# Kernel optimization log

Hardware: AMD Instinct MI355X
Metric: run time of the kernel (lower is better)

The kernel has to match this reference:

```python
import jax, jax.numpy as jnp
import numpy as np

K_BITS = 128  # hash bits (k in __init__)
WORD = 32     # pack bits into uint32 words -> K_BITS // WORD = 4 words


def _pack_bits(bits_u32):
    # bits_u32: [N, K_BITS] uint32 in {0,1} -> [N, K_BITS//WORD] uint32 keys
    N = bits_u32.shape[0]
    b = bits_u32.reshape(N, K_BITS // WORD, WORD)
    shifts = jnp.arange(WORD, dtype=jnp.uint32)
    return jnp.sum(jnp.left_shift(b, shifts), axis=-1, dtype=jnp.uint32)  # [N, 4]


def setup_inputs() -> dict:
    key = jax.random.key(0)
    k1, k2 = jax.random.split(key)
    T, B, D = 128, 64, 4096
    latent_state = jax.random.normal(k1, (T, B, D), dtype=jnp.float32)
    A = jax.random.normal(k2, (K_BITS, D), dtype=jnp.float32)  # fixed random projection buffer
    return {"latent_state": latent_state, "A": A}


def reference(latent_state, A):
    # latent_state: [T, B, D]; A: [k, D]. Returns intrinsic reward [T, B].
    T, B, D = latent_state.shape
    flat = latent_state.reshape(T * B, D)                    # detach is a no-op for fwd
    proj = flat @ A.T                                        # [N, k]
    bits = (proj > 0).astype(jnp.uint32)                     # SimHash sign bits
    words = _pack_bits(bits)                                 # [N, 4] collision-free 128-bit key

    # counts dict starts empty each run: visit count of row i is the number of
    # rows j <= i with an identical key (keys processed in row order).
    N = words.shape[0]
    eq = jnp.ones((N, N), dtype=bool)
    for w in range(K_BITS // WORD):  # small fixed loop over 4 key words
        eq = eq & (words[:, None, w] == words[None, :, w])
    counts = jnp.tril(eq).sum(axis=1)                        # [N] int, >= 1
    intrinsic = 1.0 / jnp.sqrt(counts.astype(latent_state.dtype))
    return intrinsic.reshape(T, B)
```

## Files before the change

### kernel.cpp

```cpp
#include <hip/hip_runtime.h>
#include <stdint.h>

#define D_DIM 4096
#define N_ROWS 8192

typedef __attribute__((ext_vector_type(8))) short bfrag8;
typedef __attribute__((ext_vector_type(4))) float facc4;
typedef unsigned long long u64;

__device__ __forceinline__ uint32_t pack_bf16x2(float lo, float hi) {
    union { float f; uint32_t u; } a, b;
    a.f = lo; b.f = hi;
    return (b.u & 0xFFFF0000u) | (a.u >> 16);
}

__global__ void __launch_bounds__(256)
prep_A(const float* __restrict__ A, uint32_t* __restrict__ A_sw) {
    const int S = blockIdx.x * 256 + threadIdx.x;
    const int c = S >> 10;
    const int s = S & 1023;
    const int n = s >> 3;
    const int g = (s & 7) ^ (n & 7);
    const float* src = A + (size_t)n * D_DIM + c * 64 + g * 8;
    float4 f0 = *(const float4*)(src);
    float4 f1 = *(const float4*)(src + 4);
    uint4 o;
    o.x = pack_bf16x2(f0.x, f0.y);
    o.y = pack_bf16x2(f0.z, f0.w);
    o.z = pack_bf16x2(f1.x, f1.y);
    o.w = pack_bf16x2(f1.z, f1.w);
    *(uint4*)(A_sw + (size_t)S * 4) = o;
}

__global__ void __launch_bounds__(512)
gemm_pack_n4(const float* __restrict__ L, const uint32_t* __restrict__ A_sw,
             u64* __restrict__ folded) {
    __shared__ ushort Ls[16 * 72];
    __shared__ uint4  As[1024];
    __shared__ ushort sl[8][16];

    const int tid  = threadIdx.x;
    const int wave = tid >> 6;
    const int lane = tid & 63;
    const int row0 = blockIdx.x * 16;
    const int c = lane & 15;
    const int q = lane >> 4;
    const int g  = wave >> 1;
    const int wn = wave & 1;
    const int ncol = 32 * g + 16 * wn + c;

    const int srow = (tid >> 4) & 15;
    const int sf4  = tid & 15;
    const float* lsrc = L + (size_t)(row0 + srow) * D_DIM + sf4 * 4;
    ushort* ldst = &Ls[srow * 72 + sf4 * 4];
    const bool do_ls = (tid < 256);

    facc4 acc = (facc4){0.f, 0.f, 0.f, 0.f};

    for (int kc = 0; kc < D_DIM; kc += 64) {
        const uint32_t* gA = A_sw + (size_t)(kc >> 6) * 4096;
#pragma unroll
        for (int i = 0; i < 2; i++) {
            const int slot0 = wave * 128 + i * 64;
            __builtin_amdgcn_global_load_lds(
                (const __attribute__((address_space(1))) uint32_t*)(gA + (slot0 + lane) * 4),
                (__attribute__((address_space(3))) uint32_t*)(&As[slot0]),
                16, 0, 0);
        }
        if (do_ls) {
            float4 f = *(const float4*)(lsrc + kc);
            *(uint2*)ldst = make_uint2(pack_bf16x2(f.x, f.y), pack_bf16x2(f.z, f.w));
        }
        __syncthreads();

#pragma unroll
        for (int ks = 0; ks < 2; ks++) {
            bfrag8 a = *(const bfrag8*)&Ls[c * 72 + ks * 32 + q * 8];
            const int gl = ks * 4 + q;
            bfrag8 b = *(const bfrag8*)&As[ncol * 8 + (gl ^ (ncol & 7))];
            acc = __builtin_amdgcn_mfma_f32_16x16x32_bf16(a, b, acc, 0, 0, 0);
        }
        __syncthreads();
    }

    u64 masks[4];
#pragma unroll
    for (int r = 0; r < 4; r++)
        masks[r] = __ballot(acc[r] > 0.0f);

    if (lane < 16) {
        const int qq = lane >> 2, r = lane & 3;
        sl[wave][lane] = (ushort)((masks[r] >> (16 * qq)) & 0xFFFFull);
    }
    __syncthreads();
    if (tid < 16) {
        u64 lo = (u64)sl[0][tid] | ((u64)sl[1][tid] << 16) |
                 ((u64)sl[2][tid] << 32) | ((u64)sl[3][tid] << 48);
        u64 hi = (u64)sl[4][tid] | ((u64)sl[5][tid] << 16) |
                 ((u64)sl[6][tid] << 32) | ((u64)sl[7][tid] << 48);
        folded[row0 + tid] = lo ^ hi;
    }
}

__global__ void __launch_bounds__(512)
count_rows(const u64* __restrict__ folded, float* __restrict__ out) {
    __shared__ u64 K[N_ROWS];
    const int tid = threadIdx.x;
    for (int i = tid; i < N_ROWS; i += 512) K[i] = folded[i];
    __syncthreads();

    const int g    = blockIdx.x * 8 + (tid >> 6);
    const int lane = tid & 63;
    int rows[4];
    u64 my[4];
    int cnt[4] = {0, 0, 0, 0};
#pragma unroll
    for (int r = 0; r < 4; r++) {
        rows[r] = g + 2048 * r;
        my[r] = K[rows[r]];
    }
    const int maxrow = rows[3];
    for (int j = lane; j <= maxrow; j += 64) {
        u64 k = K[j];
#pragma unroll
        for (int r = 0; r < 4; r++)
            cnt[r] += (int)((j <= rows[r]) & (k == my[r]));
    }
#pragma unroll
    for (int r = 0; r < 4; r++) {
        int v = cnt[r];
#pragma unroll
        for (int o = 32; o; o >>= 1) v += __shfl_xor(v, o, 64);
        if (lane == 0) out[rows[r]] = rsqrtf((float)v);
    }
}

extern "C" void kernel_launch(void* const* d_in, const int* in_sizes, int n_in,
                              void* d_out, int out_size, void* d_ws, size_t ws_size,
                              hipStream_t stream) {
    const float* latent = (const float*)d_in[0];
    const float* A      = (const float*)d_in[1];
    float* out          = (float*)d_out;

    uint32_t* A_sw = (uint32_t*)d_ws;
    u64* folded = (u64*)((char*)d_ws + (1 << 20));

    prep_A<<<256, 256, 0, stream>>>(A, A_sw);
    gemm_pack_n4<<<512, 512, 0, stream>>>(latent, A_sw, folded);
    count_rows<<<256, 512, 0, stream>>>(folded, out);
}
```

Before: 236.1 us.

## Split GEMM K across waves with direct global fragment loads and LDS reduction

Replaces the LDS-staged, barrier-per-chunk GEMM with a split-K scheme. Each of four waves owns a quarter of D and loads its A (latent) fragments straight from global memory with a three-stage register prefetch. It reads pre-swizzled B fragments directly from global memory and accumulates all 128 output columns in eight accumulators. Partial sums are reduced through LDS at the end before the sign-bit ballot packing. This removes per-iteration __syncthreads and LDS staging, at the cost of more registers, uncoalesced-ish direct B loads from L2, and a final reduction pass.

```diff
diff --git a/kernel.cpp b/kernel.cpp
--- a/kernel.cpp
+++ b/kernel.cpp
@@ -7,6 +7,8 @@
 typedef __attribute__((ext_vector_type(8))) short bfrag8;
 typedef __attribute__((ext_vector_type(4))) float facc4;
 typedef unsigned long long u64;
+
+union ABfrag { uint32_t u[4]; bfrag8 b; };
 
 __device__ __forceinline__ uint32_t pack_bf16x2(float lo, float hi) {
     union { float f; uint32_t u; } a, b;
@@ -32,73 +34,105 @@
     *(uint4*)(A_sw + (size_t)S * 4) = o;
 }
 
-__global__ void __launch_bounds__(512)
-gemm_pack_n4(const float* __restrict__ L, const uint32_t* __restrict__ A_sw,
-             u64* __restrict__ folded) {
-    __shared__ ushort Ls[16 * 72];
-    __shared__ uint4  As[1024];
-    __shared__ ushort sl[8][16];
+__global__ void __launch_bounds__(256, 2)
+gemm_pack_direct(const float* __restrict__ L, const uint32_t* __restrict__ A_sw,
+                 u64* __restrict__ folded) {
+    __shared__ facc4 red[3 * 512];
 
     const int tid  = threadIdx.x;
-    const int wave = tid >> 6;
+    const int w    = tid >> 6;
     const int lane = tid & 63;
     const int row0 = blockIdx.x * 16;
     const int c = lane & 15;
     const int q = lane >> 4;
-    const int g  = wave >> 1;
-    const int wn = wave & 1;
-    const int ncol = 32 * g + 16 * wn + c;
 
-    const int srow = (tid >> 4) & 15;
-    const int sf4  = tid & 15;
-    const float* lsrc = L + (size_t)(row0 + srow) * D_DIM + sf4 * 4;
-    ushort* ldst = &Ls[srow * 72 + sf4 * 4];
-    const bool do_ls = (tid < 256);
+    const float* Lrow = L + (size_t)(row0 + c) * D_DIM + w * 1024 + q * 8;
+    const uint32_t* gB0 = A_sw + (size_t)(w * 16) * 4096 + c * 32;
+    const int sw0 = (q ^ (c & 7)) * 4;
+    const int sw1 = ((4 + q) ^ (c & 7)) * 4;
 
-    facc4 acc = (facc4){0.f, 0.f, 0.f, 0.f};
+    facc4 acc[8];
+#pragma unroll
+    for (int i = 0; i < 8; i++) acc[i] = (facc4){0.f, 0.f, 0.f, 0.f};
 
-    for (int kc = 0; kc < D_DIM; kc += 64) {
-        const uint32_t* gA = A_sw + (size_t)(kc >> 6) * 4096;
+    float4 lp[4][4];
 #pragma unroll
-        for (int i = 0; i < 2; i++) {
-            const int slot0 = wave * 128 + i * 64;
-            __builtin_amdgcn_global_load_lds(
-                (const __attribute__((address_space(1))) uint32_t*)(gA + (slot0 + lane) * 4),
-                (__attribute__((address_space(3))) uint32_t*)(&As[slot0]),
-                16, 0, 0);
-        }
-        if (do_ls) {
-            float4 f = *(const float4*)(lsrc + kc);
-            *(uint2*)ldst = make_uint2(pack_bf16x2(f.x, f.y), pack_bf16x2(f.z, f.w));
-        }
-        __syncthreads();
+    for (int t = 0; t < 3; t++) {
+        const float* p = Lrow + t * 64;
+        lp[t][0] = *(const float4*)(p);
+        lp[t][1] = *(const float4*)(p + 4);
+        lp[t][2] = *(const float4*)(p + 32);
+        lp[t][3] = *(const float4*)(p + 36);
+    }
 
 #pragma unroll
-        for (int ks = 0; ks < 2; ks++) {
-            bfrag8 a = *(const bfrag8*)&Ls[c * 72 + ks * 32 + q * 8];
-            const int gl = ks * 4 + q;
-            bfrag8 b = *(const bfrag8*)&As[ncol * 8 + (gl ^ (ncol & 7))];
-            acc = __builtin_amdgcn_mfma_f32_16x16x32_bf16(a, b, acc, 0, 0, 0);
+    for (int t = 0; t < 16; t++) {
+        if (t + 3 < 16) {
+            const int s = (t + 3) & 3;
+            const float* p = Lrow + (t + 3) * 64;
+            lp[s][0] = *(const float4*)(p);
+            lp[s][1] = *(const float4*)(p + 4);
+            lp[s][2] = *(const float4*)(p + 32);
+            lp[s][3] = *(const float4*)(p + 36);
         }
-        __syncthreads();
+        const int s = t & 3;
+        const uint32_t* gB = gB0 + t * 4096;
+
+        ABfrag a0, a1;
+        a0.u[0] = pack_bf16x2(lp[s][0].x, lp[s][0].y);
+        a0.u[1] = pack_bf16x2(lp[s][0].z, lp[s][0].w);
+        a0.u[2] = pack_bf16x2(lp[s][1].x, lp[s][1].y);
+        a0.u[3] = pack_bf16x2(lp[s][1].z, lp[s][1].w);
+        a1.u[0] = pack_bf16x2(lp[s][2].x, lp[s][2].y);
+        a1.u[1] = pack_bf16x2(lp[s][2].z, lp[s][2].w);
+        a1.u[2] = pack_bf16x2(lp[s][3].x, lp[s][3].y);
+        a1.u[3] = pack_bf16x2(lp[s][3].z, lp[s][3].w);
+
+#pragma unroll
+        for (int ct = 0; ct < 8; ct++) {
+            bfrag8 b0 = *(const bfrag8*)(gB + ct * 512 + sw0);
+            acc[ct] = __builtin_amdgcn_mfma_f32_16x16x32_bf16(a0.b, b0, acc[ct], 0, 0, 0);
+        }
+#pragma unroll
+        for (int ct = 0; ct < 8; ct++) {
+            bfrag8 b1 = *(const bfrag8*)(gB + ct * 512 + sw1);
+            acc[ct] = __builtin_amdgcn_mfma_f32_16x16x32_bf16(a1.b, b1, acc[ct], 0, 0, 0);
+        }
     }
 
-    u64 masks[4];
+    const int sw = (lane >> 1) & 7;
+    if (w > 0) {
+        facc4* dst = red + (w - 1) * 512;
 #pragma unroll
-    for (int r = 0; r < 4; r++)
-        masks[r] = __ballot(acc[r] > 0.0f);
-
-    if (lane < 16) {
-        const int qq = lane >> 2, r = lane & 3;
-        sl[wave][lane] = (ushort)((masks[r] >> (16 * qq)) & 0xFFFFull);
+        for (int ct = 0; ct < 8; ct++)
+            dst[(lane * 8 + ct) ^ sw] = acc[ct];
     }
     __syncthreads();
-    if (tid < 16) {
-        u64 lo = (u64)sl[0][tid] | ((u64)sl[1][tid] << 16) |
-                 ((u64)sl[2][tid] << 32) | ((u64)sl[3][tid] << 48);
-        u64 hi = (u64)sl[4][tid] | ((u64)sl[5][tid] << 16) |
-                 ((u64)sl[6][tid] << 32) | ((u64)sl[7][tid] << 48);
-        folded[row0 + tid] = lo ^ hi;
+    if (w == 0) {
+#pragma unroll
+        for (int sidx = 0; sidx < 3; sidx++) {
+            const facc4* src = red + sidx * 512;
+#pragma unroll
+            for (int ct = 0; ct < 8; ct++)
+                acc[ct] += src[(lane * 8 + ct) ^ sw];
+        }
+        u64 lo = 0, hi = 0;
+        const int rq = lane >> 2;
+        const int rr = lane & 3;
+#pragma unroll
+        for (int ct = 0; ct < 8; ct++) {
+#pragma unroll
+            for (int r = 0; r < 4; r++) {
+                u64 m = __ballot(acc[ct][r] > 0.0f);
+                if (rr == r) {
+                    u64 sl = (m >> (16 * rq)) & 0xFFFFull;
+                    if (ct < 4) lo |= sl << (16 * ct);
+                    else        hi |= sl << (16 * (ct - 4));
+                }
+            }
+        }
+        if (lane < 16)
+            folded[row0 + lane] = lo ^ hi;
     }
 }
 
@@ -146,6 +180,6 @@
     u64* folded = (u64*)((char*)d_ws + (1 << 20));
 
     prep_A<<<256, 256, 0, stream>>>(A, A_sw);
-    gemm_pack_n4<<<512, 512, 0, stream>>>(latent, A_sw, folded);
+    gemm_pack_direct<<<512, 256, 0, stream>>>(latent, A_sw, folded);
     count_rows<<<256, 512, 0, stream>>>(folded, out);
 }
```

After: 254.3 us. 7.7% more time.
